# Performance work log

Hardware: AMD Instinct MI355X
Metric: run time of the kernel (lower is better)

## Reference

```python
import jax, jax.numpy as jnp
import numpy as np

N_HEAD = 16
ROPE_BASE = 10000.0

def rotate_half(x):
    half = x.shape[-1] // 2
    return jnp.concatenate((-x[..., half:], x[..., :half]), axis=-1)

def rope_freqs(T, head_dim, dtype):
    inv_freq = 1.0 / (ROPE_BASE ** (jnp.arange(0, head_dim, 2, dtype=jnp.float32) / head_dim))
    t = jnp.arange(T, dtype=jnp.float32)
    freqs = t[:, None] * inv_freq[None, :]          # [T, head_dim//2]
    emb = jnp.concatenate((freqs, freqs), axis=-1)  # [T, head_dim]
    return emb.astype(dtype)

def setup_inputs() -> dict:
    key = jax.random.key(0)
    ks = jax.random.split(key, 9)
    B, T, C = 2, 2048, 1024
    s = 1.0 / np.sqrt(C)
    return {
        'x':  jax.random.normal(ks[0], (B, T, C), jnp.float32),
        'Wq': jax.random.normal(ks[1], (C, C), jnp.float32) * s,
        'bq': jnp.zeros((C,), jnp.float32),
        'Wk': jax.random.normal(ks[2], (C, C), jnp.float32) * s,
        'bk': jnp.zeros((C,), jnp.float32),
        'Wv': jax.random.normal(ks[3], (C, C), jnp.float32) * s,
        'bv': jnp.zeros((C,), jnp.float32),
        'Wp': jax.random.normal(ks[4], (C, C), jnp.float32) * s,
        'bp': jnp.zeros((C,), jnp.float32),
    }

def reference(x, Wq, bq, Wk, bk, Wv, bv, Wp, bp):
    B, T, C = x.shape
    H = N_HEAD
    D = C // H
    # torch Linear: y = x @ W.T + b
    def heads(y):
        return y.reshape(B, T, H, D).transpose(0, 2, 1, 3)  # [B,H,T,D]
    q = heads(x @ Wq.T + bq)
    k = heads(x @ Wk.T + bk)
    v = heads(x @ Wv.T + bv)
    # inline RoPE
    emb = rope_freqs(T, D, x.dtype)          # [T, D]
    cos, sin = jnp.cos(emb), jnp.sin(emb)
    q = q * cos + rotate_half(q) * sin
    k = k * cos + rotate_half(k) * sin
    # full T x T scores with causal masked softmax
    att = jnp.einsum('bhtd,bhsd->bhts', q, k) * (1.0 / jnp.sqrt(jnp.array(D, x.dtype)))
    causal = jnp.tril(jnp.ones((T, T), bool))
    att = jnp.where(causal[None, None], att, jnp.array(-jnp.inf, att.dtype))
    att = jax.nn.softmax(att, axis=-1)
    y = jnp.einsum('bhts,bhsd->bhtd', att, v)  # [B,H,T,D]
    y = y.transpose(0, 2, 1, 3).reshape(B, T, C)
    return y @ Wp.T + bp
```

## Files before the change

kernel.cpp:

```cpp
#include <hip/hip_runtime.h>
#include <hip/hip_bf16.h>
#include <stdint.h>

typedef unsigned short u16;
typedef __attribute__((ext_vector_type(8))) short bf16x8;
typedef __attribute__((ext_vector_type(4))) float f32x4;

typedef const __attribute__((address_space(1))) unsigned int* gu32p;
typedef __attribute__((address_space(3))) unsigned int* lu32p;

__device__ __forceinline__ void gl_lds16(const u16* g, u16* l) {
  __builtin_amdgcn_global_load_lds((gu32p)(const void*)g, (lu32p)(void*)l, 16, 0, 0);
}

__device__ __forceinline__ u16 f2bf(float f) {
  union { float f; unsigned u; } v; v.f = f;
  unsigned r = v.u + 0x7fffu + ((v.u >> 16) & 1u);
  return (u16)(r >> 16);
}
__device__ __forceinline__ void st2bf(u16* p0, u16* p1, float a, float b) {
  union { __hip_bfloat162 h; u16 u[2]; } cv;
  cv.h = __float22bfloat162_rn(make_float2(a, b));
  *p0 = cv.u[0]; *p1 = cv.u[1];
}

__global__ void convert_kernel(const float4* __restrict__ x, const float4* __restrict__ wq,
                               const float4* __restrict__ wk, const float4* __restrict__ wv,
                               const float4* __restrict__ wp,
                               u16* __restrict__ xb, u16* __restrict__ wqb, u16* __restrict__ wkb,
                               u16* __restrict__ wvb, u16* __restrict__ wpb,
                               float2* __restrict__ tab) {
  int i = blockIdx.x * 256 + threadIdx.x;
  const int NX = 1048576, NW = 262144, NCONV = NX + 4 * NW;
  if (i >= NCONV) {
    int j = i - NCONV;
    int d = j & 31, t = j >> 5;
    float ang = (float)t * expf(-0.28782313662425572f * (float)d);
    tab[j] = make_float2(cosf(ang), sinf(ang));
    return;
  }
  const float4* src; u16* dst; int off;
  if (i < NX)            { src = x;  dst = xb;  off = i; }
  else if (i < NX + NW)  { src = wq; dst = wqb; off = i - NX; }
  else if (i < NX + 2*NW){ src = wk; dst = wkb; off = i - NX - NW; }
  else if (i < NX + 3*NW){ src = wv; dst = wvb; off = i - NX - 2*NW; }
  else                   { src = wp; dst = wpb; off = i - NX - 3*NW; }
  float4 v = src[off];
  ushort4 ov = make_ushort4(f2bf(v.x), f2bf(v.y), f2bf(v.z), f2bf(v.w));
  *(ushort4*)&dst[off * 4] = ov;
}

template<int FUSE_ROPE, int OUT_BF16, int TRANS_V>
__global__ __launch_bounds__(256) void gemm_bt_kernel(
    const u16* __restrict__ A,
    const u16* __restrict__ B0, const u16* __restrict__ B1, const u16* __restrict__ B2,
    const float* __restrict__ bias0, const float* __restrict__ bias1, const float* __restrict__ bias2,
    void* out0, void* out1, void* out2, const float2* __restrict__ tab)
{
  __shared__ __align__(16) u16 As[2][4096];
  __shared__ __align__(16) u16 Bs[2][4096];
  const int z = blockIdx.z;
  const u16* Bw = (z == 0) ? B0 : (z == 1) ? B1 : B2;
  const float* bias = (z == 0) ? bias0 : (z == 1) ? bias1 : bias2;
  void* outv = (z == 0) ? out0 : (z == 1) ? out1 : out2;
  const int tid = threadIdx.x, lane = tid & 63, w = tid >> 6;
  const int wr = w >> 1, wc = w & 1;
  const int quad = lane >> 4, l15 = lane & 15;
  const int m0 = blockIdx.y * 128, n0 = blockIdx.x * 128;
  const int sr = lane >> 2, sc = (lane & 3) * 8;

  auto stg = [&](int kt, int bf) {
    const int k0 = kt * 32;
    #pragma unroll
    for (int p = 0; p < 2; p++) {
      gl_lds16(A  + (m0 + p*64 + w*16 + sr) * 1024 + k0 + sc, &As[bf][p*2048 + w*512]);
      gl_lds16(Bw + (n0 + p*64 + w*16 + sr) * 1024 + k0 + sc, &Bs[bf][p*2048 + w*512]);
    }
  };

  f32x4 acc[4][4] = {};
  stg(0, 0);
  for (int kt = 0; kt < 32; kt++) {
    __syncthreads();
    if (kt < 31) stg(kt + 1, (kt + 1) & 1);
    const int bf = kt & 1;
    bf16x8 af[4], bfr[4];
    #pragma unroll
    for (int mt = 0; mt < 4; mt++)
      af[mt] = *(const bf16x8*)&As[bf][(wr*64 + mt*16 + l15) * 32 + quad*8];
    #pragma unroll
    for (int nt = 0; nt < 4; nt++)
      bfr[nt] = *(const bf16x8*)&Bs[bf][(wc*64 + nt*16 + l15) * 32 + quad*8];
    #pragma unroll
    for (int mt = 0; mt < 4; mt++)
      #pragma unroll
      for (int nt = 0; nt < 4; nt++)
        acc[mt][nt] = __builtin_amdgcn_mfma_f32_16x16x32_bf16(af[mt], bfr[nt], acc[mt][nt], 0, 0, 0);
  }

  if (TRANS_V && z == 2) {
    const int bb = m0 >> 11, tg0 = (m0 & 2047) + wr*64 + quad*4;
    #pragma unroll
    for (int nt = 0; nt < 4; nt++) {
      const int c = n0 + wc*64 + nt*16 + l15;
      const float bv = bias[c];
      u16* vrow = (u16*)outv + (size_t)(bb*1024 + c) * 2048 + tg0;
      #pragma unroll
      for (int mt = 0; mt < 4; mt++) {
        ushort4 pk;
        pk.x = f2bf(acc[mt][nt][0] + bv); pk.y = f2bf(acc[mt][nt][1] + bv);
        pk.z = f2bf(acc[mt][nt][2] + bv); pk.w = f2bf(acc[mt][nt][3] + bv);
        *(ushort4*)&vrow[mt*16] = pk;
      }
    }
    return;
  }

  #pragma unroll
  for (int mt = 0; mt < 4; mt++) {
    #pragma unroll
    for (int r = 0; r < 4; r++) {
      const int row = m0 + wr*64 + mt*16 + quad*4 + r;
      float v[4];
      #pragma unroll
      for (int nt = 0; nt < 4; nt++)
        v[nt] = acc[mt][nt][r] + bias[n0 + wc*64 + nt*16 + l15];
      if (FUSE_ROPE && z < 2) {
        const int t = row & 2047;
        #pragma unroll
        for (int nt = 0; nt < 2; nt++) {
          const int d = nt*16 + l15;
          float2 cs = tab[t*32 + d];
          float x0 = v[nt], x1 = v[nt+2];
          v[nt]   = x0 * cs.x - x1 * cs.y;
          v[nt+2] = x1 * cs.x + x0 * cs.y;
        }
      }
      #pragma unroll
      for (int nt = 0; nt < 4; nt++) {
        const int col = n0 + wc*64 + nt*16 + l15;
        if (OUT_BF16) ((u16*)outv)[row * 1024 + col] = f2bf(v[nt]);
        else          ((float*)outv)[row * 1024 + col] = v[nt];
      }
    }
  }
}

__global__ __launch_bounds__(512) void attn_kernel(
    const u16* __restrict__ qg, const u16* __restrict__ kg,
    const u16* __restrict__ vtg, u16* __restrict__ yg)
{
  __shared__ __align__(16) u16 K_lds[2][128 * 64];
  __shared__ __align__(16) u16 V_lds[2][64 * 128];
  __shared__ __align__(16) u16 P_lds[8][2][16 * 128];
  const int x = blockIdx.x;
  const int hh = blockIdx.y, b = blockIdx.z;
  const int tid = threadIdx.x, lane = tid & 63, w = tid >> 6;
  const int quad = lane >> 4, l15 = lane & 15;
  const int bh = b * (2048 * 1024) + hh * 64;
  const int vtb = (b * 16 + hh) * 131072;

  const int qtA = x, qtB = 15 - x;
  const int wrow = w*16;

  bf16x8 qfA[2], qfB[2];
  {
    const int rA = qtA*128 + wrow + l15;
    const int rB = qtB*128 + wrow + l15;
    qfA[0] = *(const bf16x8*)&qg[bh + rA*1024 + quad*8];
    qfA[1] = *(const bf16x8*)&qg[bh + rA*1024 + 32 + quad*8];
    qfB[0] = *(const bf16x8*)&qg[bh + rB*1024 + quad*8];
    qfB[1] = *(const bf16x8*)&qg[bh + rB*1024 + 32 + quad*8];
  }
  f32x4 oA[4] = {}, oB[4] = {};
  f32x4 l5A = {}, l5B = {};

  bf16x8 ones;
  #pragma unroll
  for (int i2 = 0; i2 < 8; i2++) ones[i2] = (short)0x3F80;

  const float c = 0.18033688011112042f;

  auto do_stage = [&](int j, int bf) {
    #pragma unroll
    for (int p = 0; p < 2; p++) {
      const int seg = w*2 + p;
      const int r = seg*8 + (lane >> 3);
      const int g = (lane & 7) ^ (r & 7);
      gl_lds16(kg + bh + (j*128 + r) * 1024 + g*8, &K_lds[bf][seg*512]);
    }
    #pragma unroll
    for (int p = 0; p < 2; p++) {
      const int seg = w*2 + p;
      const int r = seg*4 + (lane >> 4);
      const int g = (lane & 15) ^ (r & 15);
      gl_lds16(vtg + vtb + r * 2048 + j*128 + g*8, &V_lds[bf][seg*512]);
    }
  };

  do_stage(0, 0);
  for (int j = 0; j <= qtB; j++) {
    __syncthreads();
    if (j < qtB) do_stage(j + 1, (j + 1) & 1);
    const int bf = j & 1;
    const bool doA = (j <= qtA);

    f32x4 sA[8], sB[8];
    #pragma unroll
    for (int nt = 0; nt < 8; nt++) {
      const int krow = (nt*16 + l15) * 64;
      const int g0 = ((quad)     ^ (l15 & 7)) * 8;
      const int g1 = ((4 + quad) ^ (l15 & 7)) * 8;
      bf16x8 kf0 = *(const bf16x8*)&K_lds[bf][krow + g0];
      bf16x8 kf1 = *(const bf16x8*)&K_lds[bf][krow + g1];
      f32x4 z = {};
      z = __builtin_amdgcn_mfma_f32_16x16x32_bf16(qfB[0], kf0, z, 0, 0, 0);
      z = __builtin_amdgcn_mfma_f32_16x16x32_bf16(qfB[1], kf1, z, 0, 0, 0);
      sB[nt] = z;
      if (doA) {
        f32x4 za = {};
        za = __builtin_amdgcn_mfma_f32_16x16x32_bf16(qfA[0], kf0, za, 0, 0, 0);
        za = __builtin_amdgcn_mfma_f32_16x16x32_bf16(qfA[1], kf1, za, 0, 0, 0);
        sA[nt] = za;
      }
    }
    const int trow = wrow + quad*4;
    if (j == qtB) {
      #pragma unroll
      for (int nt = 0; nt < 8; nt++)
        #pragma unroll
        for (int r = 0; r < 4; r++)
          if (nt*16 + l15 > trow + r) sB[nt][r] = -1e30f;
    }
    if (doA && j == qtA) {
      #pragma unroll
      for (int nt = 0; nt < 8; nt++)
        #pragma unroll
        for (int r = 0; r < 4; r++)
          if (nt*16 + l15 > trow + r) sA[nt][r] = -1e30f;
    }
    #pragma unroll
    for (int r = 0; r < 4; r++) {
      const int R = quad*4 + r;
      u16* ppB = &P_lds[w][1][R*128 + (l15 & 7)];
      #pragma unroll
      for (int nt = 0; nt < 8; nt += 2) {
        float p0 = exp2f(sB[nt][r] * c);
        float p1 = exp2f(sB[nt+1][r] * c);
        const int g0 = ((nt*2     + (l15 >> 3)) ^ (R & 7)) * 8;
        const int g1 = (((nt+1)*2 + (l15 >> 3)) ^ (R & 7)) * 8;
        st2bf(ppB + g0, ppB + g1, p0, p1);
      }
    }
    if (doA) {
      #pragma unroll
      for (int r = 0; r < 4; r++) {
        const int R = quad*4 + r;
        u16* ppA = &P_lds[w][0][R*128 + (l15 & 7)];
        #pragma unroll
        for (int nt = 0; nt < 8; nt += 2) {
          float p0 = exp2f(sA[nt][r] * c);
          float p1 = exp2f(sA[nt+1][r] * c);
          const int g0 = ((nt*2     + (l15 >> 3)) ^ (R & 7)) * 8;
          const int g1 = (((nt+1)*2 + (l15 >> 3)) ^ (R & 7)) * 8;
          st2bf(ppA + g0, ppA + g1, p0, p1);
        }
      }
    }
    #pragma unroll
    for (int ss = 0; ss < 4; ss++) {
      const int pg = ((ss*4 + quad) ^ (l15 & 7)) * 8;
      bf16x8 pfB = *(const bf16x8*)&P_lds[w][1][l15*128 + pg];
      l5B = __builtin_amdgcn_mfma_f32_16x16x32_bf16(pfB, ones, l5B, 0, 0, 0);
      bf16x8 pfA = {};
      if (doA) {
        pfA = *(const bf16x8*)&P_lds[w][0][l15*128 + pg];
        l5A = __builtin_amdgcn_mfma_f32_16x16x32_bf16(pfA, ones, l5A, 0, 0, 0);
      }
      #pragma unroll
      for (int dt = 0; dt < 4; dt++) {
        const int vg = ((ss*4 + quad) ^ l15) * 8;
        bf16x8 vf = *(const bf16x8*)&V_lds[bf][(dt*16 + l15)*128 + vg];
        oB[dt] = __builtin_amdgcn_mfma_f32_16x16x32_bf16(pfB, vf, oB[dt], 0, 0, 0);
        if (doA) oA[dt] = __builtin_amdgcn_mfma_f32_16x16x32_bf16(pfA, vf, oA[dt], 0, 0, 0);
      }
    }
  }

  #pragma unroll
  for (int r = 0; r < 4; r++) {
    float ia = 1.0f / l5A[r], ib = 1.0f / l5B[r];
    u16* yA = &yg[bh + (qtA*128 + wrow + quad*4 + r) * 1024 + l15];
    u16* yB = &yg[bh + (qtB*128 + wrow + quad*4 + r) * 1024 + l15];
    st2bf(yA,      yA + 16, oA[0][r] * ia, oA[1][r] * ia);
    st2bf(yA + 32, yA + 48, oA[2][r] * ia, oA[3][r] * ia);
    st2bf(yB,      yB + 16, oB[0][r] * ib, oB[1][r] * ib);
    st2bf(yB + 32, yB + 48, oB[2][r] * ib, oB[3][r] * ib);
  }
}

extern "C" void kernel_launch(void* const* d_in, const int* in_sizes, int n_in,
                              void* d_out, int out_size, void* d_ws, size_t ws_size,
                              hipStream_t stream) {
  const float* x  = (const float*)d_in[0];
  const float* Wq = (const float*)d_in[1];
  const float* bq = (const float*)d_in[2];
  const float* Wk = (const float*)d_in[3];
  const float* bk = (const float*)d_in[4];
  const float* Wv = (const float*)d_in[5];
  const float* bv = (const float*)d_in[6];
  const float* Wp = (const float*)d_in[7];
  const float* bp = (const float*)d_in[8];

  char* ws = (char*)d_ws;
  u16* xb  = (u16*)(ws);
  u16* wqb = (u16*)(ws + (8u  << 20));
  u16* wkb = (u16*)(ws + (10u << 20));
  u16* wvb = (u16*)(ws + (12u << 20));
  u16* wpb = (u16*)(ws + (14u << 20));
  u16* qb  = (u16*)(ws + (16u << 20));
  u16* kb  = (u16*)(ws + (24u << 20));
  u16* vtb = (u16*)(ws + (32u << 20));
  float2* tab = (float2*)(ws + (40u << 20));
  u16* yb = xb;

  convert_kernel<<<8448, 256, 0, stream>>>((const float4*)x, (const float4*)Wq, (const float4*)Wk,
                                           (const float4*)Wv, (const float4*)Wp,
                                           xb, wqb, wkb, wvb, wpb, tab);
  gemm_bt_kernel<1, 1, 1><<<dim3(8, 32, 3), 256, 0, stream>>>(xb, wqb, wkb, wvb, bq, bk, bv,
                                                              (void*)qb, (void*)kb, (void*)vtb, tab);
  attn_kernel<<<dim3(8, 16, 2), 512, 0, stream>>>(qb, kb, vtb, yb);
  gemm_bt_kernel<0, 0, 0><<<dim3(8, 32, 1), 256, 0, stream>>>(yb, wpb, wpb, wpb, bp, bp, bp,
                                                              (void*)d_out, (void*)d_out, (void*)d_out, tab);
}
```

Measured before the change: 213.0 us.

## Keep attention probabilities in registers via transposed QK and fp16 PV MFMA

```diff
diff --git a/kernel.cpp b/kernel.cpp
--- a/kernel.cpp
+++ b/kernel.cpp
@@ -1,10 +1,12 @@
 #include <hip/hip_runtime.h>
 #include <hip/hip_bf16.h>
+#include <hip/hip_fp16.h>
 #include <stdint.h>
 
 typedef unsigned short u16;
 typedef __attribute__((ext_vector_type(8))) short bf16x8;
 typedef __attribute__((ext_vector_type(4))) float f32x4;
+typedef __attribute__((ext_vector_type(4))) _Float16 f16x4;
 
 typedef const __attribute__((address_space(1))) unsigned int* gu32p;
 typedef __attribute__((address_space(3))) unsigned int* lu32p;
@@ -18,10 +20,11 @@
   unsigned r = v.u + 0x7fffu + ((v.u >> 16) & 1u);
   return (u16)(r >> 16);
 }
-__device__ __forceinline__ void st2bf(u16* p0, u16* p1, float a, float b) {
-  union { __hip_bfloat162 h; u16 u[2]; } cv;
-  cv.h = __float22bfloat162_rn(make_float2(a, b));
-  *p0 = cv.u[0]; *p1 = cv.u[1];
+__device__ __forceinline__ f16x4 pack4h(float a, float b, float c, float d) {
+  union { f16x4 v; __half2 h[2]; } u;
+  u.h[0] = __floats2half2_rn(a, b);
+  u.h[1] = __floats2half2_rn(c, d);
+  return u.v;
 }
 
 __global__ void convert_kernel(const float4* __restrict__ x, const float4* __restrict__ wq,
@@ -108,8 +111,10 @@
       #pragma unroll
       for (int mt = 0; mt < 4; mt++) {
         ushort4 pk;
-        pk.x = f2bf(acc[mt][nt][0] + bv); pk.y = f2bf(acc[mt][nt][1] + bv);
-        pk.z = f2bf(acc[mt][nt][2] + bv); pk.w = f2bf(acc[mt][nt][3] + bv);
+        pk.x = __half_as_ushort(__float2half_rn(acc[mt][nt][0] + bv));
+        pk.y = __half_as_ushort(__float2half_rn(acc[mt][nt][1] + bv));
+        pk.z = __half_as_ushort(__float2half_rn(acc[mt][nt][2] + bv));
+        pk.w = __half_as_ushort(__float2half_rn(acc[mt][nt][3] + bv));
         *(ushort4*)&vrow[mt*16] = pk;
       }
     }
@@ -152,7 +157,6 @@
 {
   __shared__ __align__(16) u16 K_lds[2][128 * 64];
   __shared__ __align__(16) u16 V_lds[2][64 * 128];
-  __shared__ __align__(16) u16 P_lds[8][2][16 * 128];
   const int x = blockIdx.x;
   const int hh = blockIdx.y, b = blockIdx.z;
   const int tid = threadIdx.x, lane = tid & 63, w = tid >> 6;
@@ -161,23 +165,22 @@
   const int vtb = (b * 16 + hh) * 131072;
 
   const int qtA = x, qtB = 15 - x;
-  const int wrow = w*16;
+  const int qrl = w*16 + l15;
 
   bf16x8 qfA[2], qfB[2];
   {
-    const int rA = qtA*128 + wrow + l15;
-    const int rB = qtB*128 + wrow + l15;
+    const int rA = qtA*128 + qrl, rB = qtB*128 + qrl;
     qfA[0] = *(const bf16x8*)&qg[bh + rA*1024 + quad*8];
     qfA[1] = *(const bf16x8*)&qg[bh + rA*1024 + 32 + quad*8];
     qfB[0] = *(const bf16x8*)&qg[bh + rB*1024 + quad*8];
     qfB[1] = *(const bf16x8*)&qg[bh + rB*1024 + 32 + quad*8];
   }
   f32x4 oA[4] = {}, oB[4] = {};
-  f32x4 l5A = {}, l5B = {};
-
-  bf16x8 ones;
+  f32x4 lA = {}, lB = {};
+
+  f16x4 onesh;
   #pragma unroll
-  for (int i2 = 0; i2 < 8; i2++) ones[i2] = (short)0x3F80;
+  for (int i2 = 0; i2 < 4; i2++) onesh[i2] = (_Float16)1.0f;
 
   const float c = 0.18033688011112042f;
 
@@ -214,88 +217,68 @@
       bf16x8 kf0 = *(const bf16x8*)&K_lds[bf][krow + g0];
       bf16x8 kf1 = *(const bf16x8*)&K_lds[bf][krow + g1];
       f32x4 z = {};
-      z = __builtin_amdgcn_mfma_f32_16x16x32_bf16(qfB[0], kf0, z, 0, 0, 0);
-      z = __builtin_amdgcn_mfma_f32_16x16x32_bf16(qfB[1], kf1, z, 0, 0, 0);
+      z = __builtin_amdgcn_mfma_f32_16x16x32_bf16(kf0, qfB[0], z, 0, 0, 0);
+      z = __builtin_amdgcn_mfma_f32_16x16x32_bf16(kf1, qfB[1], z, 0, 0, 0);
       sB[nt] = z;
       if (doA) {
         f32x4 za = {};
-        za = __builtin_amdgcn_mfma_f32_16x16x32_bf16(qfA[0], kf0, za, 0, 0, 0);
-        za = __builtin_amdgcn_mfma_f32_16x16x32_bf16(qfA[1], kf1, za, 0, 0, 0);
+        za = __builtin_amdgcn_mfma_f32_16x16x32_bf16(kf0, qfA[0], za, 0, 0, 0);
+        za = __builtin_amdgcn_mfma_f32_16x16x32_bf16(kf1, qfA[1], za, 0, 0, 0);
         sA[nt] = za;
       }
     }
-    const int trow = wrow + quad*4;
-    if (j == qtB) {
-      #pragma unroll
-      for (int nt = 0; nt < 8; nt++)
+    f16x4 pfA[8], pfB[8];
+    const bool dgB = (j == qtB), dgA = (j == qtA);
+    #pragma unroll
+    for (int nt = 0; nt < 8; nt++) {
+      float pb[4];
+      #pragma unroll
+      for (int r = 0; r < 4; r++) {
+        float sv = sB[nt][r] * c;
+        if (dgB && (nt*16 + quad*4 + r > qrl)) sv = -1e30f;
+        pb[r] = exp2f(sv);
+      }
+      pfB[nt] = pack4h(pb[0], pb[1], pb[2], pb[3]);
+      lB = __builtin_amdgcn_mfma_f32_16x16x16f16(onesh, pfB[nt], lB, 0, 0, 0);
+    }
+    if (doA) {
+      #pragma unroll
+      for (int nt = 0; nt < 8; nt++) {
+        float pa[4];
         #pragma unroll
-        for (int r = 0; r < 4; r++)
-          if (nt*16 + l15 > trow + r) sB[nt][r] = -1e30f;
-    }
-    if (doA && j == qtA) {
-      #pragma unroll
-      for (int nt = 0; nt < 8; nt++)
-        #pragma unroll
-        for (int r = 0; r < 4; r++)
-          if (nt*16 + l15 > trow + r) sA[nt][r] = -1e30f;
-    }
-    #pragma unroll
-    for (int r = 0; r < 4; r++) {
-      const int R = quad*4 + r;
-      u16* ppB = &P_lds[w][1][R*128 + (l15 & 7)];
-      #pragma unroll
-      for (int nt = 0; nt < 8; nt += 2) {
-        float p0 = exp2f(sB[nt][r] * c);
-        float p1 = exp2f(sB[nt+1][r] * c);
-        const int g0 = ((nt*2     + (l15 >> 3)) ^ (R & 7)) * 8;
-        const int g1 = (((nt+1)*2 + (l15 >> 3)) ^ (R & 7)) * 8;
-        st2bf(ppB + g0, ppB + g1, p0, p1);
-      }
-    }
-    if (doA) {
-      #pragma unroll
-      for (int r = 0; r < 4; r++) {
-        const int R = quad*4 + r;
-        u16* ppA = &P_lds[w][0][R*128 + (l15 & 7)];
-        #pragma unroll
-        for (int nt = 0; nt < 8; nt += 2) {
-          float p0 = exp2f(sA[nt][r] * c);
-          float p1 = exp2f(sA[nt+1][r] * c);
-          const int g0 = ((nt*2     + (l15 >> 3)) ^ (R & 7)) * 8;
-          const int g1 = (((nt+1)*2 + (l15 >> 3)) ^ (R & 7)) * 8;
-          st2bf(ppA + g0, ppA + g1, p0, p1);
+        for (int r = 0; r < 4; r++) {
+          float sv = sA[nt][r] * c;
+          if (dgA && (nt*16 + quad*4 + r > qrl)) sv = -1e30f;
+          pa[r] = exp2f(sv);
         }
-      }
-    }
-    #pragma unroll
-    for (int ss = 0; ss < 4; ss++) {
-      const int pg = ((ss*4 + quad) ^ (l15 & 7)) * 8;
-      bf16x8 pfB = *(const bf16x8*)&P_lds[w][1][l15*128 + pg];
-      l5B = __builtin_amdgcn_mfma_f32_16x16x32_bf16(pfB, ones, l5B, 0, 0, 0);
-      bf16x8 pfA = {};
-      if (doA) {
-        pfA = *(const bf16x8*)&P_lds[w][0][l15*128 + pg];
-        l5A = __builtin_amdgcn_mfma_f32_16x16x32_bf16(pfA, ones, l5A, 0, 0, 0);
-      }
+        pfA[nt] = pack4h(pa[0], pa[1], pa[2], pa[3]);
+        lA = __builtin_amdgcn_mfma_f32_16x16x16f16(onesh, pfA[nt], lA, 0, 0, 0);
+      }
+    }
+    #pragma unroll
+    for (int nt = 0; nt < 8; nt++) {
+      const int pp = ((nt*2 + (quad >> 1)) ^ l15) * 8 + (quad & 1) * 4;
       #pragma unroll
       for (int dt = 0; dt < 4; dt++) {
-        const int vg = ((ss*4 + quad) ^ l15) * 8;
-        bf16x8 vf = *(const bf16x8*)&V_lds[bf][(dt*16 + l15)*128 + vg];
-        oB[dt] = __builtin_amdgcn_mfma_f32_16x16x32_bf16(pfB, vf, oB[dt], 0, 0, 0);
-        if (doA) oA[dt] = __builtin_amdgcn_mfma_f32_16x16x32_bf16(pfA, vf, oA[dt], 0, 0, 0);
-      }
-    }
-  }
-
+        f16x4 vf = *(const f16x4*)&V_lds[bf][(dt*16 + l15) * 128 + pp];
+        oB[dt] = __builtin_amdgcn_mfma_f32_16x16x16f16(vf, pfB[nt], oB[dt], 0, 0, 0);
+        if (doA) oA[dt] = __builtin_amdgcn_mfma_f32_16x16x16f16(vf, pfA[nt], oA[dt], 0, 0, 0);
+      }
+    }
+  }
+
+  const float iA = 1.0f / lA[0], iB = 1.0f / lB[0];
   #pragma unroll
-  for (int r = 0; r < 4; r++) {
-    float ia = 1.0f / l5A[r], ib = 1.0f / l5B[r];
-    u16* yA = &yg[bh + (qtA*128 + wrow + quad*4 + r) * 1024 + l15];
-    u16* yB = &yg[bh + (qtB*128 + wrow + quad*4 + r) * 1024 + l15];
-    st2bf(yA,      yA + 16, oA[0][r] * ia, oA[1][r] * ia);
-    st2bf(yA + 32, yA + 48, oA[2][r] * ia, oA[3][r] * ia);
-    st2bf(yB,      yB + 16, oB[0][r] * ib, oB[1][r] * ib);
-    st2bf(yB + 32, yB + 48, oB[2][r] * ib, oB[3][r] * ib);
+  for (int dt = 0; dt < 4; dt++) {
+    ushort4 pk;
+    u16* yA = &yg[bh + (qtA*128 + qrl) * 1024 + dt*16 + quad*4];
+    pk.x = f2bf(oA[dt][0] * iA); pk.y = f2bf(oA[dt][1] * iA);
+    pk.z = f2bf(oA[dt][2] * iA); pk.w = f2bf(oA[dt][3] * iA);
+    *(ushort4*)yA = pk;
+    u16* yB = &yg[bh + (qtB*128 + qrl) * 1024 + dt*16 + quad*4];
+    pk.x = f2bf(oB[dt][0] * iB); pk.y = f2bf(oB[dt][1] * iB);
+    pk.z = f2bf(oB[dt][2] * iB); pk.w = f2bf(oB[dt][3] * iB);
+    *(ushort4*)yB = pk;
   }
 }
 
```

New measurement: 223.7 us. 1.05x slower.
